# Kernel tuning notes

Measured on AMD Instinct MI355X. Metric: run time of the kernel, lower is better.

The kernel has to match this reference:

```python
import jax, jax.numpy as jnp
import numpy as np
from jax import lax

# ---- config (mirrors cfg) ----
NUM_LEVELS = 4
DS = 2            # DS_FACTOR
T = 16            # TILE_SIZE
SR = 4            # SEARCH_RADIUS
PADD = 1
SW = 0.1          # SPATIAL_WEIGHT
GR = 2            # GAUSS_RADIUS
SIGMA = 1.0
SS = 2 * (SR + PADD) + 1      # 11: padded search grid
SSC = 2 * SR + 1              # 9: cropped search grid
WIN = T + 2 * (SR + PADD)     # 26: gathered window per tile

# ---- subpixel-refinement quadratic-fit filters (from __init__) ----
F_A11 = jnp.asarray(np.array([[1,-2,1],[2,-4,2],[1,-2,1]], np.float32) / 4.0)
F_A22 = jnp.asarray(np.array([[1,2,1],[-2,-4,-2],[1,2,1]], np.float32) / 4.0)
F_A12 = jnp.asarray(np.array([[1,0,-1],[0,0,0],[-1,0,1]], np.float32) / 4.0)
F_B1  = jnp.asarray(np.array([[-1,0,1],[-2,0,2],[-1,0,1]], np.float32) / 8.0)
F_B2  = jnp.asarray(np.array([[-1,-2,-1],[0,0,0],[1,2,1]], np.float32) / 8.0)
F_C   = jnp.asarray(np.array([[-1,2,-1],[2,12,2],[-1,2,-1]], np.float32) / 16.0)


def _gauss_kernel():
    ws = 2 * GR + 1
    ax = np.arange(ws, dtype=np.float32) - GR
    g = np.exp(-(ax ** 2) / (2.0 * SIGMA ** 2))
    k = np.outer(g, g)
    k = k / k.sum()
    return jnp.asarray(k, jnp.float32)


def _pyramid(x):
    """Gaussian pyramid: depthwise gaussian blur + avg-pool(ds) per level."""
    k = _gauss_kernel()[None, None]  # OIHW, C=1
    pad = (2 * GR + 1 - 1) // 2
    pyr = [x]
    for _ in range(NUM_LEVELS - 1):
        y = lax.conv_general_dilated(x, k, (1, 1), [(pad, pad), (pad, pad)],
                                     dimension_numbers=('NCHW', 'OIHW', 'NCHW'))
        n, c, h, w = y.shape
        x = y.reshape(n, c, h // DS, DS, w // DS, DS).mean(axis=(3, 5))
        pyr.append(x)
    return pyr


def _sdist_map():
    ax = (np.arange(SS, dtype=np.float32) - (SR + PADD)) / float(SS)
    return jnp.asarray(ax[:, None] ** 2 + ax[None, :] ** 2, jnp.float32)


def _step(init_offset, src, dst):
    """One pyramid-level block-matching step + subpixel refine."""
    n, nth, ntw, _ = init_offset.shape
    H, W = src.shape[2], src.shape[3]
    oy = jnp.round(init_offset[..., 0]).astype(jnp.int32)
    ox = jnp.round(init_offset[..., 1]).astype(jnp.int32)
    base_y = (jnp.arange(nth, dtype=jnp.int32) * T)[None, :, None]
    base_x = (jnp.arange(ntw, dtype=jnp.int32) * T)[None, None, :]
    y0 = base_y + oy - (SR + PADD)
    x0 = base_x + ox - (SR + PADD)
    Y = jnp.clip(y0[..., None] + jnp.arange(WIN), 0, H - 1)
    X = jnp.clip(x0[..., None] + jnp.arange(WIN), 0, W - 1)
    nidx = jnp.arange(n)[:, None, None, None, None]
    window = dst[:, 0][nidx, Y[..., :, None], X[..., None, :]]
    # source tiles [n,nth,ntw,T,T]
    src_t = src[:, 0].reshape(n, nth, T, ntw, T).transpose(0, 1, 3, 2, 4)
    # all SSxSS candidate tiles from the window (static slide indices)
    sl = jnp.arange(SS)[:, None] + jnp.arange(T)[None, :]  # [SS,T]
    cand = window[:, :, :, sl[:, None, :, None], sl[None, :, None, :]]  # [n,nth,ntw,SS,SS,T,T]
    adist = jnp.mean((cand - src_t[:, :, :, None, None]) ** 2, axis=(-2, -1))
    dist_full = adist + SW * _sdist_map()  # [n,nth,ntw,SS,SS]
    dist = dist_full[:, :, :, PADD:-PADD, PADD:-PADD].reshape(n, nth, ntw, SSC * SSC)
    min_dist = jnp.min(dist, axis=3)
    pk = jnp.argmin(dist, axis=3)
    py = pk // SSC
    px = pk % SSC
    offset = init_offset + jnp.stack([(py - SR).astype(jnp.float32),
                                      (px - SR).astype(jnp.float32)], axis=3)
    # RegionSelection: 3x3 neighborhood of dist_full around (py+PADD, px+PADD)
    ry = (py + PADD)[..., None] + jnp.arange(-1, 2)
    rx = (px + PADD)[..., None] + jnp.arange(-1, 2)
    tyi = jnp.arange(nth)[None, :, None, None, None]
    txi = jnp.arange(ntw)[None, None, :, None, None]
    yreg = dist_full[nidx, tyi, txi, ry[..., :, None], rx[..., None, :]]  # [n,nth,ntw,3,3]
    s = lambda f: jnp.sum(f * yreg, axis=(-2, -1))
    a11 = jax.nn.relu(s(F_A11))
    a22 = jax.nn.relu(s(F_A22))
    a12 = s(F_A12)
    b1 = s(F_B1)
    b2 = s(F_B2)
    det = a11 * a22 - a12 ** 2
    a12z = jnp.where(det < 0, jnp.zeros_like(a12), a12)
    mu_x = -(a22 * b1 - a12z * b2) / det
    mu_y = -(a11 * b2 - a12z * b1) / det
    mu_len = jnp.sqrt(mu_y ** 2 + mu_x ** 2)
    dx = jnp.where(mu_len < 1.0, mu_x, jnp.zeros_like(mu_x))
    dy = jnp.where(mu_len < 1.0, mu_y, jnp.zeros_like(mu_y))
    offset = offset.at[..., 0].add(dy).at[..., 1].add(dx)
    return offset, min_dist


def _inherit(prev_offset, nth, ntw, H, W):
    typ = jnp.arange(nth) // DS
    txp = jnp.arange(ntw) // DS
    off = DS * prev_offset[:, typ[:, None], txp[None, :], :]
    iy = (jnp.arange(nth, dtype=jnp.float32) * T)[None, :, None]
    ix = (jnp.arange(ntw, dtype=jnp.float32) * T)[None, None, :]
    dy = jnp.clip(off[..., 0] + iy, 0.0, float(H - T)) - iy
    dx = jnp.clip(off[..., 1] + ix, 0.0, float(W - T)) - ix
    return jnp.round(jnp.stack([dy, dx], axis=3))


def _align(src, dst):
    ps = _pyramid(src)
    pd = _pyramid(dst)
    offset = None
    min_dist = None
    for level in range(NUM_LEVELS - 1, -1, -1):
        s, d = ps[level], pd[level]
        n, _, h, w = s.shape
        nth = int(np.ceil(h / T))
        ntw = int(np.ceil(w / T))
        if level == NUM_LEVELS - 1:
            init = jnp.zeros((n, nth, ntw, 2), jnp.float32)
        else:
            init = _inherit(offset, nth, ntw, h, w)
        offset, min_dist = _step(init, s, d)
    # nearest-neighbor upsample by TILE_SIZE to per-pixel maps
    pixel_off = jnp.repeat(jnp.repeat(offset, T, axis=1), T, axis=2)   # [n,H,W,2]
    pixel_dist = jnp.repeat(jnp.repeat(min_dist, T, axis=1), T, axis=2)  # [n,H,W]
    return pixel_off, pixel_dist


def setup_inputs() -> dict:
    key = jax.random.key(0)
    k1, k2 = jax.random.split(key)
    src = jax.random.uniform(k1, (4, 1, 512, 512), jnp.float32)
    dst = jax.random.uniform(k2, (4, 1, 512, 512), jnp.float32)
    return {"src": src, "dst": dst}


def reference(src, dst):
    return _align(src, dst)
```

## Files before the change

### kernel.cpp

```cpp
#include <hip/hip_runtime.h>


#define NB 4
#define NPIX (NB * 512 * 512)
#define OFFS_BASE 1212416

constexpr float H6[6] = {
    0.027244342f, 0.149345013f, 0.323410645f,
    0.323410645f, 0.149345013f, 0.027244342f
};

__global__ void __launch_bounds__(256, 4)
pyramid_kernel(const float* __restrict__ src, const float* __restrict__ dst,
               float* __restrict__ ws) {
    __shared__ float smem[8160];
    float* patch = smem;
    float* tmpH1 = smem + 5520;
    float* l1    = smem;
    float* tmpH2 = smem + 1232;
    float* l2    = smem + 1792;
    float* tmpH3 = smem + 2032;

    float* sL1 = ws;
    float* dL1 = sL1 + 4 * 65536;
    float* sL2 = dL1 + 4 * 65536;
    float* dL2 = sL2 + 4 * 16384;
    float* sL3 = dL2 + 4 * 16384;
    float* dL3 = sL3 + 4 * 4096;

    const int bx = blockIdx.x, by = blockIdx.y, z = blockIdx.z;
    const int t = threadIdx.x;
    const float* in = (z < 4) ? (src + (size_t)z * 262144) : (dst + (size_t)(z - 4) * 262144);
    float* oL1 = ((z < 4) ? sL1 : dL1) + (size_t)(z & 3) * 65536;
    float* oL2 = ((z < 4) ? sL2 : dL2) + (size_t)(z & 3) * 16384;
    float* oL3 = ((z < 4) ? sL3 : dL3) + (size_t)(z & 3) * 4096;

    {
        const int oy = by * 32 - 14, ox = bx * 64 - 14;
        for (int idx = t; idx < 5520; idx += 256) {
            int r = idx / 92, c = idx - r * 92;
            int gy = oy + r, gx = ox + c;
            float v = 0.f;
            if ((unsigned)gy < 512u && (unsigned)gx < 512u) v = in[gy * 512 + gx];
            patch[r * 92 + c] = v;
        }
    }
    __syncthreads();
    for (int idx = t; idx < 2640; idx += 256) {
        int r = idx / 44, v = idx - r * 44;
        const float* p = &patch[r * 92 + 2 * v];
        float a = 0.f;
        #pragma unroll
        for (int bq = 0; bq < 6; ++bq) a = fmaf(H6[bq], p[bq], a);
        tmpH1[r * 44 + v] = a;
    }
    __syncthreads();
    {
        const int oy = by * 16 - 6, ox = bx * 32 - 6;
        for (int idx = t; idx < 1232; idx += 256) {
            int u = idx / 44, v = idx - u * 44;
            float a = 0.f;
            int y1 = oy + u, x1 = ox + v;
            if ((unsigned)y1 < 256u && (unsigned)x1 < 256u) {
                #pragma unroll
                for (int bq = 0; bq < 6; ++bq) a = fmaf(H6[bq], tmpH1[(2 * u + bq) * 44 + v], a);
            }
            l1[u * 44 + v] = a;
        }
    }
    __syncthreads();
    {
        #pragma unroll
        for (int k = 0; k < 2; ++k) {
            int idx = t + k * 256;
            int u = idx >> 5, v = idx & 31;
            oL1[(by * 16 + u) * 256 + bx * 32 + v] = l1[(6 + u) * 44 + 6 + v];
        }
    }
    for (int idx = t; idx < 560; idx += 256) {
        int r = idx / 20, v = idx - r * 20;
        const float* p = &l1[r * 44 + 2 * v];
        float a = 0.f;
        #pragma unroll
        for (int bq = 0; bq < 6; ++bq) a = fmaf(H6[bq], p[bq], a);
        tmpH2[r * 20 + v] = a;
    }
    __syncthreads();
    {
        const int oy = by * 8 - 2, ox = bx * 16 - 2;
        if (t < 240) {
            int u = t / 20, v = t - u * 20;
            float a = 0.f;
            int y2 = oy + u, x2 = ox + v;
            if ((unsigned)y2 < 128u && (unsigned)x2 < 128u) {
                #pragma unroll
                for (int bq = 0; bq < 6; ++bq) a = fmaf(H6[bq], tmpH2[(2 * u + bq) * 20 + v], a);
            }
            l2[u * 20 + v] = a;
        }
    }
    __syncthreads();
    if (t < 128) {
        int u = t >> 4, v = t & 15;
        oL2[(by * 8 + u) * 128 + bx * 16 + v] = l2[(2 + u) * 20 + 2 + v];
    } else if (t < 224) {
        int idx = t - 128;
        int r = idx >> 3, v = idx & 7;
        const float* p = &l2[r * 20 + 2 * v];
        float a = 0.f;
        #pragma unroll
        for (int bq = 0; bq < 6; ++bq) a = fmaf(H6[bq], p[bq], a);
        tmpH3[r * 8 + v] = a;
    }
    __syncthreads();
    if (t < 32) {
        int u = t >> 3, v = t & 7;
        float a = 0.f;
        #pragma unroll
        for (int bq = 0; bq < 6; ++bq) a = fmaf(H6[bq], tmpH3[(2 * u + bq) * 8 + v], a);
        oL3[(by * 4 + u) * 64 + bx * 8 + v] = a;
    }
}

__device__ __forceinline__ void inherit_off(int ty, int tx, int H,
                                            float pary, float parx,
                                            float& dyf, float& dxf) {
    float iy = (float)(ty * 16), ix = (float)(tx * 16);
    dyf = rintf(fminf(fmaxf(2.f * pary + iy, 0.f), (float)(H - 16)) - iy);
    dxf = rintf(fminf(fmaxf(2.f * parx + ix, 0.f), (float)(H - 16)) - ix);
}

template<int NL>
__device__ __forceinline__ void load_win(const float* __restrict__ dimg, int H,
                                         int y0, int x0, float* win, int lt) {
    const int c = lt & 31;
    const int r0 = lt >> 5;
    constexpr int RSTEP = NL / 32;
    if (c < 26) {
        const int gx = min(max(x0 + c, 0), H - 1);
        #pragma unroll
        for (int k = 0; k < (26 + RSTEP - 1) / RSTEP; ++k) {
            const int rr = r0 + k * RSTEP;
            if (rr < 26) {
                const int gy = min(max(y0 + rr, 0), H - 1);
                win[rr * 28 + c] = dimg[gy * H + gx];
            }
        }
    }
}

template<bool FULL>
__device__ __forceinline__ void ssd_dist(const float* win, const float* st,
                                         float* dist, int lt) {
    const int dy = FULL ? (lt >> 4) : (lt >> 3);
    if (dy < 11) {
        float acc[11];
        #pragma unroll
        for (int q = 0; q < 11; ++q) acc[q] = 0.f;
        constexpr int ROWS = FULL ? 1 : 2;
        #pragma unroll
        for (int rr = 0; rr < ROWS; ++rr) {
            const int i = FULL ? (lt & 15) : ((lt & 7) * 2 + rr);
            float w[28], s[16];
            const float4* wp = (const float4*)&win[(dy + i) * 28];
            #pragma unroll
            for (int q = 0; q < 7; ++q) ((float4*)w)[q] = wp[q];
            const float4* sp = (const float4*)&st[i * 20];
            #pragma unroll
            for (int q = 0; q < 4; ++q) ((float4*)s)[q] = sp[q];
            #pragma unroll
            for (int dx = 0; dx < 11; ++dx) {
                #pragma unroll
                for (int j = 0; j < 16; ++j) {
                    float d = w[dx + j] - s[j];
                    acc[dx] = fmaf(d, d, acc[dx]);
                }
            }
        }
        constexpr int MMAX = FULL ? 8 : 4;
        #pragma unroll
        for (int m = 1; m <= MMAX; m <<= 1) {
            #pragma unroll
            for (int dx = 0; dx < 11; ++dx) acc[dx] += __shfl_xor(acc[dx], m);
        }
        const bool leader = FULL ? ((lt & 15) == 0) : ((lt & 7) == 0);
        if (leader) {
            float ay = (float)(dy - 5) * (1.f / 11.f);
            #pragma unroll
            for (int dx = 0; dx < 11; ++dx) {
                float ax = (float)(dx - 5) * (1.f / 11.f);
                dist[dy * 11 + dx] = acc[dx] * (1.f / 256.f) + 0.1f * (ay * ay + ax * ax);
            }
        }
    }
}

__device__ __forceinline__ void argmin_refine(const float* dist, int lt,
                                              float dyf, float dxf,
                                              float& roy, float& rox, float& rod) {
    const int l = lt & 63;
    float bv; int bk;
    {
        int k = l;
        int py = k / 9, px = k - (k / 9) * 9;
        bv = dist[(py + 1) * 11 + (px + 1)]; bk = k;
        k = l + 64;
        if (k < 81) {
            py = k / 9; px = k - (k / 9) * 9;
            float d = dist[(py + 1) * 11 + (px + 1)];
            if (d < bv) { bv = d; bk = k; }
        }
    }
    #pragma unroll
    for (int m = 1; m <= 32; m <<= 1) {
        float ov = __shfl_xor(bv, m);
        int   ok = __shfl_xor(bk, m);
        if (ov < bv || (ov == bv && ok < bk)) { bv = ov; bk = ok; }
    }
    {
        int py = bk / 9, px = bk - (bk / 9) * 9;
        float y00 = dist[(py + 0) * 11 + (px + 0)], y01 = dist[(py + 0) * 11 + (px + 1)], y02 = dist[(py + 0) * 11 + (px + 2)];
        float y10 = dist[(py + 1) * 11 + (px + 0)], y11 = dist[(py + 1) * 11 + (px + 1)], y12 = dist[(py + 1) * 11 + (px + 2)];
        float y20 = dist[(py + 2) * 11 + (px + 0)], y21 = dist[(py + 2) * 11 + (px + 1)], y22 = dist[(py + 2) * 11 + (px + 2)];

        float a11 = (y00 - 2.f * y01 + y02 + 2.f * y10 - 4.f * y11 + 2.f * y12 + y20 - 2.f * y21 + y22) * 0.25f;
        a11 = fmaxf(a11, 0.f);
        float a22 = (y00 + 2.f * y01 + y02 - 2.f * y10 - 4.f * y11 - 2.f * y12 + y20 + 2.f * y21 + y22) * 0.25f;
        a22 = fmaxf(a22, 0.f);
        float a12 = (y00 - y02 - y20 + y22) * 0.25f;
        float b1  = (-y00 + y02 - 2.f * y10 + 2.f * y12 - y20 + y22) * 0.125f;
        float b2  = (-y00 - 2.f * y01 - y02 + y20 + 2.f * y21 + y22) * 0.125f;

        float det  = a11 * a22 - a12 * a12;
        float a12z = (det < 0.f) ? 0.f : a12;
        float mu_x = -(a22 * b1 - a12z * b2) / det;
        float mu_y = -(a11 * b2 - a12z * b1) / det;
        float mu_len = sqrtf(mu_x * mu_x + mu_y * mu_y);
        float addx = (mu_len < 1.f) ? mu_x : 0.f;
        float addy = (mu_len < 1.f) ? mu_y : 0.f;

        roy = dyf + (float)(py - 4) + addy;
        rox = dxf + (float)(px - 4) + addx;
        rod = bv;
    }
}

__global__ void __launch_bounds__(256, 4)
seed_kernel(const float* __restrict__ ws_ro, float* __restrict__ ws) {
    __shared__ float smem[1496];
    float* win_c  = smem;
    float* dist_c = smem + 728;
    float* stL3   = smem + 856;
    float* stL2   = smem + 1176;

    const float* sL2 = ws_ro + 4 * 65536 + 4 * 65536;
    const float* dL2 = sL2 + 4 * 16384;
    const float* sL3 = dL2 + 4 * 16384;
    const float* dL3 = sL3 + 4 * 4096;
    float* offs = ws + OFFS_BASE;

    const int gid = blockIdx.x;
    const int b   = gid >> 6;
    const int ty2 = (gid >> 3) & 7;
    const int tx2 = gid & 7;
    const int t   = threadIdx.x;

    const float* s2 = sL2 + (size_t)b * 16384;  const float* d2 = dL2 + (size_t)b * 16384;
    const float* s3 = sL3 + (size_t)b * 4096;   const float* d3 = dL3 + (size_t)b * 4096;

    {
        const int it = t & 63, r = it >> 2, q = t & 3;
        if (t < 64) {
            const float4* p = (const float4*)(s3 + (size_t)((ty2 >> 1) * 16 + r) * 64 + (tx2 >> 1) * 16);
            ((float4*)&stL3[r * 20])[q] = p[q];
        } else if (t < 128) {
            const float4* p = (const float4*)(s2 + (size_t)(ty2 * 16 + r) * 128 + tx2 * 16);
            ((float4*)&stL2[r * 20])[q] = p[q];
        }
    }

    float oy, ox, od;
    load_win<256>(d3, 64, (ty2 >> 1) * 16 - 5, (tx2 >> 1) * 16 - 5, win_c, t);
    __syncthreads();
    ssd_dist<true>(win_c, stL3, dist_c, t);
    __syncthreads();
    argmin_refine(dist_c, t, 0.f, 0.f, oy, ox, od);
    {
        float dyf, dxf; inherit_off(ty2, tx2, 128, oy, ox, dyf, dxf);
        load_win<256>(d2, 128, ty2 * 16 + (int)dyf - 5, tx2 * 16 + (int)dxf - 5, win_c, t);
        __syncthreads();
        ssd_dist<true>(win_c, stL2, dist_c, t);
        __syncthreads();
        argmin_refine(dist_c, t, dyf, dxf, oy, ox, od);
    }
    if (t == 0) {
        const int oi = ((b * 8 + ty2) * 8 + tx2) * 2;
        offs[oi]     = oy;
        offs[oi + 1] = ox;
    }
}

__global__ void __launch_bounds__(256, 4)
step_chain_kernel(const float* __restrict__ src, const float* __restrict__ dst,
                  const float* __restrict__ ws, float* __restrict__ out) {
    __shared__ float smem[5880];

    const float* sL1 = ws;
    const float* offs = ws + OFFS_BASE;

    const int gid = blockIdx.x;
    const int b   = gid >> 8;
    const int ty1 = (gid >> 4) & 15;
    const int tx1 = gid & 15;
    const int t    = threadIdx.x;
    const int slot = t >> 7;
    const int s_t  = t & 127;

    float* win_c  = smem;
    float* winA   = smem + 728 + (2 * slot + 0) * 728;
    float* winB   = smem + 728 + (2 * slot + 1) * 728;
    float* dist_c = smem + 3640;
    float* distA  = smem + 3768 + (2 * slot + 0) * 128;
    float* distB  = smem + 3768 + (2 * slot + 1) * 128;
    float* stL1 = smem + 4280;
    float* st0  = smem + 4600;

    const float* s0 = src + (size_t)b * 262144; const float* d0 = dst + (size_t)b * 262144;
    const float* s1 = sL1 + (size_t)b * 65536;
    const float* d1 = sL1 + 4 * 65536 + (size_t)b * 65536;

    const int oi = ((b * 8 + (ty1 >> 1)) * 8 + (tx1 >> 1)) * 2;
    const float poy = offs[oi], pox = offs[oi + 1];

    {
        const int it = t & 63, r = it >> 2, q = t & 3;
        const int c = t >> 6;
        const int ty0 = 2 * ty1 + (c >> 1), tx0 = 2 * tx1 + (c & 1);
        const float4* p0 = (const float4*)(s0 + (size_t)(ty0 * 16 + r) * 512 + tx0 * 16);
        ((float4*)&st0[c * 320 + r * 20])[q] = p0[q];
        if (t < 64) {
            const float4* p = (const float4*)(s1 + (size_t)(ty1 * 16 + r) * 256 + tx1 * 16);
            ((float4*)&stL1[r * 20])[q] = p[q];
        }
    }

    float oy, ox, od;
    {
        float dyf, dxf; inherit_off(ty1, tx1, 256, poy, pox, dyf, dxf);
        load_win<256>(d1, 256, ty1 * 16 + (int)dyf - 5, tx1 * 16 + (int)dxf - 5, win_c, t);
        __syncthreads();
        ssd_dist<true>(win_c, stL1, dist_c, t);
        __syncthreads();
        argmin_refine(dist_c, t, dyf, dxf, oy, ox, od);
    }

    const int tyA = 2 * ty1,     txA = 2 * tx1 + slot;
    const int tyB = 2 * ty1 + 1, txB = 2 * tx1 + slot;
    float dyfA, dxfA, dyfB, dxfB;
    inherit_off(tyA, txA, 512, oy, ox, dyfA, dxfA);
    inherit_off(tyB, txB, 512, oy, ox, dyfB, dxfB);
    load_win<128>(d0, 512, tyA * 16 + (int)dyfA - 5, txA * 16 + (int)dxfA - 5, winA, s_t);
    load_win<128>(d0, 512, tyB * 16 + (int)dyfB - 5, txB * 16 + (int)dxfB - 5, winB, s_t);
    __syncthreads();
    ssd_dist<false>(winA, st0 + (0 * 2 + slot) * 320, distA, s_t);
    __syncthreads();
    ssd_dist<false>(winB, st0 + (1 * 2 + slot) * 320, distB, s_t);
    __syncthreads();

    const int r = s_t >> 3, c2 = (s_t & 7) * 2;
    {
        float oyA, oxA, odA;
        argmin_refine(distA, s_t, dyfA, dxfA, oyA, oxA, odA);
        int pyy = tyA * 16 + r, pxx = txA * 16 + c2;
        size_t pi = ((size_t)(b * 512 + pyy)) * 512 + pxx;
        float2 o; o.x = oyA; o.y = oxA;
        ((float2*)out)[pi]     = o;
        ((float2*)out)[pi + 1] = o;
        float2 dd; dd.x = odA; dd.y = odA;
        *(float2*)(out + (size_t)NPIX * 2 + pi) = dd;
    }
    {
        float oyB, oxB, odB;
        argmin_refine(distB, s_t, dyfB, dxfB, oyB, oxB, odB);
        int pyy = tyB * 16 + r, pxx = txB * 16 + c2;
        size_t pi = ((size_t)(b * 512 + pyy)) * 512 + pxx;
        float2 o; o.x = oyB; o.y = oxB;
        ((float2*)out)[pi]     = o;
        ((float2*)out)[pi + 1] = o;
        float2 dd; dd.x = odB; dd.y = odB;
        *(float2*)(out + (size_t)NPIX * 2 + pi) = dd;
    }
}

extern "C" void kernel_launch(void* const* d_in, const int* in_sizes, int n_in,
                              void* d_out, int out_size, void* d_ws, size_t ws_size,
                              hipStream_t stream) {
    const float* src = (const float*)d_in[0];
    const float* dst = (const float*)d_in[1];
    float* out = (float*)d_out;
    float* ws  = (float*)d_ws;

    hipLaunchKernelGGL(pyramid_kernel, dim3(8, 16, 8), dim3(256), 0, stream, src, dst, ws);
    hipLaunchKernelGGL(seed_kernel, dim3(256), dim3(256), 0, stream, (const float*)ws, ws);
    hipLaunchKernelGGL(step_chain_kernel, dim3(1024), dim3(256), 0, stream, src, dst, ws, out);
}
```

Measured before the change: 102.5 us.

## Split fused level-1/level-0 step kernel into separate s1 and s0 kernels

The fused step_chain kernel ran the level-1 search and then the four child level-0 tile searches inside one 256-thread block, with two serialized SSD passes per half-block. It is now split into an s1 kernel that writes level-1 offsets to workspace and an s0 kernel that launches one 128-thread block per level-0 tile. The aim is more blocks, smaller shared memory per block and fewer serialized syncs, which should raise occupancy. The cost is an extra kernel launch and a workspace round trip for the level-1 offsets.

```diff
diff --git a/kernel.cpp b/kernel.cpp
--- a/kernel.cpp
+++ b/kernel.cpp
@@ -4,6 +4,7 @@
 #define NB 4
 #define NPIX (NB * 512 * 512)
 #define OFFS_BASE 1212416
+#define OFFS1_BASE (OFFS_BASE + 512)
 
 constexpr float H6[6] = {
     0.027244342f, 0.149345013f, 0.323410645f,
@@ -301,47 +302,33 @@
 }
 
 __global__ void __launch_bounds__(256, 4)
-step_chain_kernel(const float* __restrict__ src, const float* __restrict__ dst,
-                  const float* __restrict__ ws, float* __restrict__ out) {
-    __shared__ float smem[5880];
-
-    const float* sL1 = ws;
-    const float* offs = ws + OFFS_BASE;
+s1_kernel(const float* __restrict__ ws_ro, float* __restrict__ ws) {
+    __shared__ float smem[1176];
+    float* win_c  = smem;
+    float* dist_c = smem + 728;
+    float* stL1   = smem + 856;
+
+    const float* sL1 = ws_ro;
+    const float* dL1 = sL1 + 4 * 65536;
+    const float* offs = ws_ro + OFFS_BASE;
+    float* offs1 = ws + OFFS1_BASE;
 
     const int gid = blockIdx.x;
     const int b   = gid >> 8;
     const int ty1 = (gid >> 4) & 15;
     const int tx1 = gid & 15;
-    const int t    = threadIdx.x;
-    const int slot = t >> 7;
-    const int s_t  = t & 127;
-
-    float* win_c  = smem;
-    float* winA   = smem + 728 + (2 * slot + 0) * 728;
-    float* winB   = smem + 728 + (2 * slot + 1) * 728;
-    float* dist_c = smem + 3640;
-    float* distA  = smem + 3768 + (2 * slot + 0) * 128;
-    float* distB  = smem + 3768 + (2 * slot + 1) * 128;
-    float* stL1 = smem + 4280;
-    float* st0  = smem + 4600;
-
-    const float* s0 = src + (size_t)b * 262144; const float* d0 = dst + (size_t)b * 262144;
+    const int t   = threadIdx.x;
+
     const float* s1 = sL1 + (size_t)b * 65536;
-    const float* d1 = sL1 + 4 * 65536 + (size_t)b * 65536;
+    const float* d1 = dL1 + (size_t)b * 65536;
 
     const int oi = ((b * 8 + (ty1 >> 1)) * 8 + (tx1 >> 1)) * 2;
     const float poy = offs[oi], pox = offs[oi + 1];
 
-    {
-        const int it = t & 63, r = it >> 2, q = t & 3;
-        const int c = t >> 6;
-        const int ty0 = 2 * ty1 + (c >> 1), tx0 = 2 * tx1 + (c & 1);
-        const float4* p0 = (const float4*)(s0 + (size_t)(ty0 * 16 + r) * 512 + tx0 * 16);
-        ((float4*)&st0[c * 320 + r * 20])[q] = p0[q];
-        if (t < 64) {
-            const float4* p = (const float4*)(s1 + (size_t)(ty1 * 16 + r) * 256 + tx1 * 16);
-            ((float4*)&stL1[r * 20])[q] = p[q];
-        }
+    if (t < 64) {
+        const int r = t >> 2, q = t & 3;
+        const float4* p = (const float4*)(s1 + (size_t)(ty1 * 16 + r) * 256 + tx1 * 16);
+        ((float4*)&stL1[r * 20])[q] = p[q];
     }
 
     float oy, ox, od;
@@ -353,43 +340,59 @@
         __syncthreads();
         argmin_refine(dist_c, t, dyf, dxf, oy, ox, od);
     }
-
-    const int tyA = 2 * ty1,     txA = 2 * tx1 + slot;
-    const int tyB = 2 * ty1 + 1, txB = 2 * tx1 + slot;
-    float dyfA, dxfA, dyfB, dxfB;
-    inherit_off(tyA, txA, 512, oy, ox, dyfA, dxfA);
-    inherit_off(tyB, txB, 512, oy, ox, dyfB, dxfB);
-    load_win<128>(d0, 512, tyA * 16 + (int)dyfA - 5, txA * 16 + (int)dxfA - 5, winA, s_t);
-    load_win<128>(d0, 512, tyB * 16 + (int)dyfB - 5, txB * 16 + (int)dxfB - 5, winB, s_t);
-    __syncthreads();
-    ssd_dist<false>(winA, st0 + (0 * 2 + slot) * 320, distA, s_t);
-    __syncthreads();
-    ssd_dist<false>(winB, st0 + (1 * 2 + slot) * 320, distB, s_t);
-    __syncthreads();
-
-    const int r = s_t >> 3, c2 = (s_t & 7) * 2;
-    {
-        float oyA, oxA, odA;
-        argmin_refine(distA, s_t, dyfA, dxfA, oyA, oxA, odA);
-        int pyy = tyA * 16 + r, pxx = txA * 16 + c2;
-        size_t pi = ((size_t)(b * 512 + pyy)) * 512 + pxx;
-        float2 o; o.x = oyA; o.y = oxA;
-        ((float2*)out)[pi]     = o;
-        ((float2*)out)[pi + 1] = o;
-        float2 dd; dd.x = odA; dd.y = odA;
-        *(float2*)(out + (size_t)NPIX * 2 + pi) = dd;
-    }
-    {
-        float oyB, oxB, odB;
-        argmin_refine(distB, s_t, dyfB, dxfB, oyB, oxB, odB);
-        int pyy = tyB * 16 + r, pxx = txB * 16 + c2;
-        size_t pi = ((size_t)(b * 512 + pyy)) * 512 + pxx;
-        float2 o; o.x = oyB; o.y = oxB;
-        ((float2*)out)[pi]     = o;
-        ((float2*)out)[pi + 1] = o;
-        float2 dd; dd.x = odB; dd.y = odB;
-        *(float2*)(out + (size_t)NPIX * 2 + pi) = dd;
-    }
+    if (t == 0) {
+        const int o1 = (((b * 16) + ty1) * 16 + tx1) * 2;
+        offs1[o1]     = oy;
+        offs1[o1 + 1] = ox;
+    }
+}
+
+__global__ void __launch_bounds__(128, 4)
+s0_kernel(const float* __restrict__ src, const float* __restrict__ dst,
+          const float* __restrict__ ws, float* __restrict__ out) {
+    __shared__ float smem[1176];
+    float* win  = smem;
+    float* dist = smem + 728;
+    float* st   = smem + 856;
+
+    const float* offs1 = ws + OFFS1_BASE;
+
+    const int gid = blockIdx.x;
+    const int b   = gid >> 10;
+    const int ty0 = (gid >> 5) & 31;
+    const int tx0 = gid & 31;
+    const int t   = threadIdx.x;
+
+    const float* s0 = src + (size_t)b * 262144;
+    const float* d0 = dst + (size_t)b * 262144;
+
+    const int o1 = (((b * 16) + (ty0 >> 1)) * 16 + (tx0 >> 1)) * 2;
+    const float poy = offs1[o1], pox = offs1[o1 + 1];
+
+    if (t < 64) {
+        const int r = t >> 2, q = t & 3;
+        const float4* p = (const float4*)(s0 + (size_t)(ty0 * 16 + r) * 512 + tx0 * 16);
+        ((float4*)&st[r * 20])[q] = p[q];
+    }
+
+    float dyf, dxf;
+    inherit_off(ty0, tx0, 512, poy, pox, dyf, dxf);
+    load_win<128>(d0, 512, ty0 * 16 + (int)dyf - 5, tx0 * 16 + (int)dxf - 5, win, t);
+    __syncthreads();
+    ssd_dist<false>(win, st, dist, t);
+    __syncthreads();
+
+    float oy, ox, od;
+    argmin_refine(dist, t, dyf, dxf, oy, ox, od);
+
+    const int r = t >> 3, c2 = (t & 7) * 2;
+    int pyy = ty0 * 16 + r, pxx = tx0 * 16 + c2;
+    size_t pi = ((size_t)(b * 512 + pyy)) * 512 + pxx;
+    float2 o; o.x = oy; o.y = ox;
+    ((float2*)out)[pi]     = o;
+    ((float2*)out)[pi + 1] = o;
+    float2 dd; dd.x = od; dd.y = od;
+    *(float2*)(out + (size_t)NPIX * 2 + pi) = dd;
 }
 
 extern "C" void kernel_launch(void* const* d_in, const int* in_sizes, int n_in,
@@ -402,5 +405,6 @@
 
     hipLaunchKernelGGL(pyramid_kernel, dim3(8, 16, 8), dim3(256), 0, stream, src, dst, ws);
     hipLaunchKernelGGL(seed_kernel, dim3(256), dim3(256), 0, stream, (const float*)ws, ws);
-    hipLaunchKernelGGL(step_chain_kernel, dim3(1024), dim3(256), 0, stream, src, dst, ws, out);
-}
+    hipLaunchKernelGGL(s1_kernel, dim3(1024), dim3(256), 0, stream, (const float*)ws, ws);
+    hipLaunchKernelGGL(s0_kernel, dim3(4096), dim3(128), 0, stream, src, dst, (const float*)ws, out);
+}
```

Result: slower. 107.4 us (+4.7%).
